# Performance work log

Hardware: AMD Instinct MI355X
Metric: run time of the kernel (lower is better)

Reference implementation:

```python
import jax, jax.numpy as jnp
import numpy as np

B, T, N = 16, 1000, 100
ENC, VOCAB, EMB, HID, ATT, PROJ = 512, 10025, 640, 1024, 1024, 1024


def setup_inputs() -> dict:
    key = jax.random.key(0)
    ks = jax.random.split(key, 20)
    g = lambda k, shape, s=0.02: (jax.random.normal(k, shape) * s).astype(jnp.float32)
    inp = {
        "encoder_outputs": jax.random.normal(ks[0], (B, T, ENC), dtype=jnp.float32),
        "labels": jax.random.randint(ks[1], (B, N), 0, VOCAB),
        "enc_seq_len": jax.random.randint(ks[2], (B,), T // 2, T + 1),
        # parameters (torch layout: Linear weight [out, in])
        "embed_table": g(ks[3], (VOCAB, EMB)),
        "W_ih": g(ks[4], (4 * HID, EMB + ENC)),
        "W_hh": g(ks[5], (4 * HID, HID)),
        "b_ih": jnp.zeros((4 * HID,), jnp.float32),
        "b_hh": jnp.zeros((4 * HID,), jnp.float32),
        "W_s": g(ks[6], (ATT, HID)),              # s_transformed, no bias
        "W_enc": g(ks[7], (ATT, ENC)),            # enc_ctx
        "b_enc": jnp.zeros((ATT,), jnp.float32),
        "v_att": g(ks[8], (ATT,)),                # attention energy vector
        "W_fert": g(ks[9], (ENC,)),               # inv_fertility [1,ENC] squeezed
        "W_fb": g(ks[10], (ATT,)),                # weight_feedback [ATT,1] squeezed
        "W_ro": g(ks[11], (PROJ, HID + EMB + ENC)),
        "b_ro": jnp.zeros((PROJ,), jnp.float32),
        "W_out": g(ks[12], (VOCAB, PROJ // 2)),
        "b_out": jnp.zeros((VOCAB,), jnp.float32),
    }
    return inp


def _decode(encoder_outputs, labels, enc_seq_len, embed_table, W_ih, W_hh, b_ih,
            b_hh, W_s, W_enc, b_enc, v_att, W_fert, W_fb, W_ro, b_ro, W_out, b_out):
    Bb, Tt, _ = encoder_outputs.shape
    # shifted target embeddings: pad one zero step at front, drop last -> [B,N,EMB]
    emb = embed_table[labels]
    emb = jnp.concatenate([jnp.zeros_like(emb[:, :1]), emb[:, :-1]], axis=1)

    enc_ctx = jnp.einsum("btd,ad->bta", encoder_outputs, W_enc) + b_enc  # [B,T,ATT]
    inv_fert = jax.nn.sigmoid(encoder_outputs @ W_fert)                   # [B,T]
    seq_mask = jnp.arange(Tt)[None, :] < enc_seq_len[:, None]             # [B,T]

    def step(carry, e_t):
        h, c, att_ctx, accum = carry  # h,c:[B,HID]  att_ctx:[B,ENC]  accum:[B,T]
        x = jnp.concatenate([e_t, att_ctx], axis=-1)
        gates = x @ W_ih.T + b_ih + h @ W_hh.T + b_hh
        i, f, gg, o = jnp.split(gates, 4, axis=-1)
        c_new = jax.nn.sigmoid(f) * c + jax.nn.sigmoid(i) * jnp.tanh(gg)
        h_new = jax.nn.sigmoid(o) * jnp.tanh(c_new)

        s_t = h_new @ W_s.T                                   # [B,ATT]
        wf = accum[:, :, None] * W_fb[None, None, :]          # [B,T,ATT]
        energies = jnp.tanh(enc_ctx + s_t[:, None, :] + wf) @ v_att  # [B,T]
        energies = jnp.where(seq_mask, energies, -jnp.inf)
        weights = jax.nn.softmax(energies, axis=1)            # [B,T]
        ctx = jnp.einsum("bt,btd->bd", weights, encoder_outputs)
        accum_new = accum + weights * inv_fert * 0.5
        return (h_new, c_new, ctx, accum_new), (h_new, ctx)

    carry0 = (
        jnp.zeros((Bb, HID), jnp.float32),
        jnp.zeros((Bb, HID), jnp.float32),
        jnp.zeros((Bb, ENC), jnp.float32),
        jnp.zeros((Bb, Tt), jnp.float32),
    )
    carry, (s_seq, ctx_seq) = jax.lax.scan(step, carry0, emb.transpose(1, 0, 2))
    s_stacked = s_seq.transpose(1, 0, 2)        # [B,N,HID]
    ctx_stacked = ctx_seq.transpose(1, 0, 2)    # [B,N,ENC]

    ro_in = jnp.concatenate([s_stacked, emb, ctx_stacked], axis=-1) @ W_ro.T + b_ro
    readout = jnp.max(ro_in.reshape(Bb, ro_in.shape[1], -1, 2), axis=-1)  # maxout
    logits = readout @ W_out.T + b_out
    return logits, carry


def reference(encoder_outputs, labels, enc_seq_len, embed_table, W_ih, W_hh, b_ih,
              b_hh, W_s, W_enc, b_enc, v_att, W_fert, W_fb, W_ro, b_ro, W_out, b_out):
    logits, (h, c, att_ctx, accum) = _decode(
        encoder_outputs, labels, enc_seq_len, embed_table, W_ih, W_hh, b_ih, b_hh,
        W_s, W_enc, b_enc, v_att, W_fert, W_fb, W_ro, b_ro, W_out, b_out)
    return logits, h, c, att_ctx, accum
```

## Files before the change

kernel.cpp:

```cpp
#include <hip/hip_runtime.h>
#include <math.h>

#define Bsz 16
#define Tsz 1000
#define Nsz 100
#define ENC 512
#define VOCAB 10025
#define EMB 640
#define HID 1024
#define ATT 1024
#define KX (EMB + ENC)
#define KRO (HID + EMB + ENC)

__device__ __forceinline__ float4 ld4(const float* p) { return *reinterpret_cast<const float4*>(p); }
__device__ __forceinline__ float dot4(float4 a, float4 b) { return a.x*b.x + a.y*b.y + a.z*b.z + a.w*b.w; }
__device__ __forceinline__ float sigmoidf_(float x) { return 1.f / (1.f + __expf(-x)); }
__device__ __forceinline__ float ftanh_(float x) {
    x = fminf(15.f, fmaxf(-15.f, x));
    float e = __expf(2.f * x);
    return (e - 1.f) / (e + 1.f);
}

__global__ __launch_bounds__(256) void k_init(float* accum) {
    int i = blockIdx.x * 256 + threadIdx.x;
    if (i < Bsz * Tsz) accum[i] = 0.f;
}

__global__ __launch_bounds__(256) void k_embed(const int* __restrict__ labels,
                                               const float* __restrict__ table,
                                               float* __restrict__ roA) {
    int idx = blockIdx.x * 256 + threadIdx.x;
    if (idx >= Bsz * Nsz * EMB) return;
    int e = idx % EMB;
    int bn = idx / EMB;
    int n = bn % Nsz, b = bn / Nsz;
    float v = 0.f;
    if (n > 0) {
        int lab = labels[b * Nsz + n - 1];
        v = table[(size_t)lab * EMB + e];
    }
    roA[(size_t)bn * KRO + HID + e] = v;
}

#define BM 64
#define BN 64
#define BK 16
template <int MAXOUT>
__global__ __launch_bounds__(256) void sgemm_nt(const float* __restrict__ A,
                                                const float* __restrict__ W,
                                                const float* __restrict__ bias,
                                                float* __restrict__ C,
                                                int M, int Nc, int K, int ldC) {
    __shared__ __align__(16) float As[BK][BM + 4];
    __shared__ __align__(16) float Ws[BK][BN + 4];
    int m0 = blockIdx.y * BM, n0 = blockIdx.x * BN;
    int tid = threadIdx.x;
    int tx = tid & 15, ty = tid >> 4;
    int lr = tid >> 2;
    int lk = (tid & 3) * 4;
    float acc[4][4] = {};
    for (int k0 = 0; k0 < K; k0 += BK) {
        {
            int m = m0 + lr;
            float4 v = (m < M) ? ld4(&A[(size_t)m * K + k0 + lk]) : float4{0.f, 0.f, 0.f, 0.f};
            As[lk + 0][lr] = v.x; As[lk + 1][lr] = v.y; As[lk + 2][lr] = v.z; As[lk + 3][lr] = v.w;
        }
        {
            int n = n0 + lr;
            float4 v = (n < Nc) ? ld4(&W[(size_t)n * K + k0 + lk]) : float4{0.f, 0.f, 0.f, 0.f};
            Ws[lk + 0][lr] = v.x; Ws[lk + 1][lr] = v.y; Ws[lk + 2][lr] = v.z; Ws[lk + 3][lr] = v.w;
        }
        __syncthreads();
#pragma unroll
        for (int k = 0; k < BK; k++) {
            float4 a = *reinterpret_cast<const float4*>(&As[k][ty * 4]);
            float4 w = *reinterpret_cast<const float4*>(&Ws[k][tx * 4]);
            acc[0][0] += a.x * w.x; acc[0][1] += a.x * w.y; acc[0][2] += a.x * w.z; acc[0][3] += a.x * w.w;
            acc[1][0] += a.y * w.x; acc[1][1] += a.y * w.y; acc[1][2] += a.y * w.z; acc[1][3] += a.y * w.w;
            acc[2][0] += a.z * w.x; acc[2][1] += a.z * w.y; acc[2][2] += a.z * w.z; acc[2][3] += a.z * w.w;
            acc[3][0] += a.w * w.x; acc[3][1] += a.w * w.y; acc[3][2] += a.w * w.z; acc[3][3] += a.w * w.w;
        }
        __syncthreads();
    }
#pragma unroll
    for (int i = 0; i < 4; i++) {
        int m = m0 + ty * 4 + i;
        if (m >= M) continue;
        if (MAXOUT) {
#pragma unroll
            for (int j = 0; j < 2; j++) {
                int n = n0 + tx * 4 + 2 * j;
                float v0 = acc[i][2 * j] + bias[n];
                float v1 = acc[i][2 * j + 1] + bias[n + 1];
                C[(size_t)m * ldC + n / 2] = fmaxf(v0, v1);
            }
        } else {
#pragma unroll
            for (int j = 0; j < 4; j++) {
                int n = n0 + tx * 4 + j;
                if (n < Nc) C[(size_t)m * ldC + n] = acc[i][j] + bias[n];
            }
        }
    }
}

__global__ __launch_bounds__(256) void k_ifert(const float* __restrict__ enc,
                                               const float* __restrict__ Wfert,
                                               float* __restrict__ ifert) {
    int wv = (blockIdx.x * 256 + threadIdx.x) >> 6;
    int lane = threadIdx.x & 63;
    if (wv >= Bsz * Tsz) return;
    const float* row = enc + (size_t)wv * ENC;
    float s = 0.f;
    for (int k = lane * 4; k < ENC; k += 256) s += dot4(ld4(row + k), ld4(Wfert + k));
    for (int o = 32; o; o >>= 1) s += __shfl_xor(s, o, 64);
    if (lane == 0) ifert[wv] = 1.f / (1.f + __expf(-s));
}

__global__ __launch_bounds__(256) void k_gates(float* __restrict__ roA, float* __restrict__ cbuf,
                                               const float* __restrict__ Wih, const float* __restrict__ Whh,
                                               const float* __restrict__ bih, const float* __restrict__ bhh,
                                               int t) {
    int wv = (blockIdx.x * 256 + threadIdx.x) >> 6;
    int lane = threadIdx.x & 63;
    int j = wv >> 1;
    int b0 = (wv & 1) << 3;
    float acc[4][8];
#pragma unroll
    for (int g = 0; g < 4; g++)
#pragma unroll
        for (int bb = 0; bb < 8; bb++) acc[g][bb] = 0.f;

    const float* wi0 = Wih + (size_t)(0 * HID + j) * KX;
    const float* wi1 = Wih + (size_t)(1 * HID + j) * KX;
    const float* wi2 = Wih + (size_t)(2 * HID + j) * KX;
    const float* wi3 = Wih + (size_t)(3 * HID + j) * KX;
    const float* wh0 = Whh + (size_t)(0 * HID + j) * HID;
    const float* wh1 = Whh + (size_t)(1 * HID + j) * HID;
    const float* wh2 = Whh + (size_t)(2 * HID + j) * HID;
    const float* wh3 = Whh + (size_t)(3 * HID + j) * HID;
    const float* xrow[8];
    const float* prow[8];
#pragma unroll
    for (int bb = 0; bb < 8; bb++) {
        xrow[bb] = roA + (size_t)((b0 + bb) * Nsz + t) * KRO;
        prow[bb] = roA + (size_t)((b0 + bb) * Nsz + (t - 1)) * KRO;
    }
    for (int k = lane * 4; k < EMB; k += 256) {
        float4 w0 = ld4(wi0 + k), w1 = ld4(wi1 + k), w2 = ld4(wi2 + k), w3 = ld4(wi3 + k);
#pragma unroll
        for (int bb = 0; bb < 8; bb++) {
            float4 x = ld4(xrow[bb] + HID + k);
            acc[0][bb] += dot4(w0, x); acc[1][bb] += dot4(w1, x);
            acc[2][bb] += dot4(w2, x); acc[3][bb] += dot4(w3, x);
        }
    }
    if (t > 0) {
        for (int k = lane * 4; k < ENC; k += 256) {
            float4 w0 = ld4(wi0 + EMB + k), w1 = ld4(wi1 + EMB + k), w2 = ld4(wi2 + EMB + k), w3 = ld4(wi3 + EMB + k);
#pragma unroll
            for (int bb = 0; bb < 8; bb++) {
                float4 x = ld4(prow[bb] + HID + EMB + k);
                acc[0][bb] += dot4(w0, x); acc[1][bb] += dot4(w1, x);
                acc[2][bb] += dot4(w2, x); acc[3][bb] += dot4(w3, x);
            }
        }
        for (int k = lane * 4; k < HID; k += 256) {
            float4 w0 = ld4(wh0 + k), w1 = ld4(wh1 + k), w2 = ld4(wh2 + k), w3 = ld4(wh3 + k);
#pragma unroll
            for (int bb = 0; bb < 8; bb++) {
                float4 x = ld4(prow[bb] + k);
                acc[0][bb] += dot4(w0, x); acc[1][bb] += dot4(w1, x);
                acc[2][bb] += dot4(w2, x); acc[3][bb] += dot4(w3, x);
            }
        }
    }
#pragma unroll
    for (int g = 0; g < 4; g++)
#pragma unroll
        for (int bb = 0; bb < 8; bb++) {
            float v = acc[g][bb];
            for (int o = 32; o; o >>= 1) v += __shfl_xor(v, o, 64);
            acc[g][bb] = v;
        }
    if (lane < 8) {
        int b = b0 + lane;
        float gi = acc[0][lane] + bih[j] + bhh[j];
        float gf = acc[1][lane] + bih[HID + j] + bhh[HID + j];
        float gg = acc[2][lane] + bih[2 * HID + j] + bhh[2 * HID + j];
        float go = acc[3][lane] + bih[3 * HID + j] + bhh[3 * HID + j];
        float cold = (t > 0) ? cbuf[b * HID + j] : 0.f;
        float cn = sigmoidf_(gf) * cold + sigmoidf_(gi) * ftanh_(gg);
        float hn = sigmoidf_(go) * ftanh_(cn);
        cbuf[b * HID + j] = cn;
        roA[(size_t)(b * Nsz + t) * KRO + j] = hn;
    }
}

__global__ __launch_bounds__(256) void k_s(const float* __restrict__ roA, const float* __restrict__ Wsm,
                                           float* __restrict__ st, int t) {
    int wv = (blockIdx.x * 256 + threadIdx.x) >> 6;
    int lane = threadIdx.x & 63;
    float acc[16];
#pragma unroll
    for (int b = 0; b < 16; b++) acc[b] = 0.f;
    const float* wr = Wsm + (size_t)wv * HID;
    const float* hrow[16];
#pragma unroll
    for (int b = 0; b < 16; b++) hrow[b] = roA + (size_t)(b * Nsz + t) * KRO;
    for (int k = lane * 4; k < HID; k += 256) {
        float4 w = ld4(wr + k);
#pragma unroll
        for (int b = 0; b < 16; b++) acc[b] += dot4(w, ld4(hrow[b] + k));
    }
#pragma unroll
    for (int b = 0; b < 16; b++) {
        float v = acc[b];
        for (int o = 32; o; o >>= 1) v += __shfl_xor(v, o, 64);
        acc[b] = v;
    }
    if (lane < 16) st[lane * ATT + wv] = acc[lane];
}

__global__ __launch_bounds__(256) void k_energy(const float* __restrict__ encctx,
                                                const float* __restrict__ st,
                                                const float* __restrict__ Wfb,
                                                const float* __restrict__ vatt,
                                                const float* __restrict__ accum,
                                                const int* __restrict__ seqlen,
                                                float* __restrict__ enw) {
    int wv = (blockIdx.x * 256 + threadIdx.x) >> 6;
    int lane = threadIdx.x & 63;
    int b = wv / Tsz, t = wv - b * Tsz;
    if (t >= seqlen[b]) {
        if (lane == 0) enw[wv] = -INFINITY;
        return;
    }
    float ac = accum[wv];
    const float* ec = encctx + (size_t)wv * ATT;
    const float* sr = st + b * ATT;
    float e = 0.f;
    for (int k = lane * 4; k < ATT; k += 256) {
        float4 c4 = ld4(ec + k), s4 = ld4(sr + k), f4 = ld4(Wfb + k), v4 = ld4(vatt + k);
        e += ftanh_(c4.x + s4.x + ac * f4.x) * v4.x;
        e += ftanh_(c4.y + s4.y + ac * f4.y) * v4.y;
        e += ftanh_(c4.z + s4.z + ac * f4.z) * v4.z;
        e += ftanh_(c4.w + s4.w + ac * f4.w) * v4.w;
    }
    for (int o = 32; o; o >>= 1) e += __shfl_xor(e, o, 64);
    if (lane == 0) enw[wv] = e;
}

__global__ __launch_bounds__(256) void k_softmax(float* __restrict__ enw, const float* __restrict__ ifert,
                                                 float* __restrict__ accum, float* __restrict__ roA,
                                                 const int* __restrict__ seqlen, int tstep) {
    int b = blockIdx.x, tid = threadIdx.x;
    __shared__ float redm[4], reds[4];
    int len = seqlen[b];
    float* row = enw + b * Tsz;
    float m = -INFINITY;
    for (int t = tid; t < len; t += 256) m = fmaxf(m, row[t]);
    for (int o = 32; o; o >>= 1) m = fmaxf(m, __shfl_xor(m, o, 64));
    if ((tid & 63) == 0) redm[tid >> 6] = m;
    __syncthreads();
    float M = fmaxf(fmaxf(redm[0], redm[1]), fmaxf(redm[2], redm[3]));
    float s = 0.f;
    for (int t = tid; t < len; t += 256) s += __expf(row[t] - M);
    for (int o = 32; o; o >>= 1) s += __shfl_xor(s, o, 64);
    if ((tid & 63) == 0) reds[tid >> 6] = s;
    __syncthreads();
    float inv = 1.f / (reds[0] + reds[1] + reds[2] + reds[3]);
    for (int t = tid; t < Tsz; t += 256) {
        float w = (t < len) ? __expf(row[t] - M) * inv : 0.f;
        row[t] = w;
        accum[b * Tsz + t] += w * ifert[b * Tsz + t] * 0.5f;
    }
    for (int d = tid; d < ENC; d += 256) roA[(size_t)(b * Nsz + tstep) * KRO + HID + EMB + d] = 0.f;
}

#define TCH 10
__global__ __launch_bounds__(256) void k_ctx(const float* __restrict__ enw, const float* __restrict__ enc,
                                             const int* __restrict__ seqlen, float* __restrict__ roA,
                                             int tstep) {
    int b = blockIdx.y;
    int tid = threadIdx.x;
    int len = seqlen[b];
    int t0 = blockIdx.x * (Tsz / TCH);
    int t1 = min(t0 + Tsz / TCH, len);
    if (t0 >= t1) return;
    float a0 = 0.f, a1 = 0.f;
    const float* w = enw + b * Tsz;
    for (int t = t0; t < t1; t++) {
        float wt = w[t];
        const float* er = enc + (size_t)(b * Tsz + t) * ENC;
        a0 += wt * er[tid];
        a1 += wt * er[tid + 256];
    }
    float* dst = roA + (size_t)(b * Nsz + tstep) * KRO + HID + EMB;
    atomicAdd(dst + tid, a0);
    atomicAdd(dst + tid + 256, a1);
}

__global__ __launch_bounds__(256) void k_final(const float* __restrict__ roA, const float* __restrict__ cbuf,
                                               const float* __restrict__ accum, float* __restrict__ out) {
    int idx = blockIdx.x * 256 + threadIdx.x;
    const int base = Bsz * Nsz * VOCAB;
    const int OH = Bsz * HID, OC = Bsz * HID, OA = Bsz * ENC, OAC = Bsz * Tsz;
    if (idx < OH) {
        int b = idx / HID, j = idx % HID;
        out[base + idx] = roA[(size_t)(b * Nsz + Nsz - 1) * KRO + j];
        return;
    }
    idx -= OH;
    if (idx < OC) { out[base + OH + idx] = cbuf[idx]; return; }
    idx -= OC;
    if (idx < OA) {
        int b = idx / ENC, d = idx % ENC;
        out[base + OH + OC + idx] = roA[(size_t)(b * Nsz + Nsz - 1) * KRO + HID + EMB + d];
        return;
    }
    idx -= OA;
    if (idx < OAC) out[base + OH + OC + OA + idx] = accum[idx];
}

extern "C" void kernel_launch(void* const* d_in, const int* in_sizes, int n_in,
                              void* d_out, int out_size, void* d_ws, size_t ws_size,
                              hipStream_t stream) {
    const float* enc   = (const float*)d_in[0];
    const int* labels  = (const int*)d_in[1];
    const int* seqlen  = (const int*)d_in[2];
    const float* table = (const float*)d_in[3];
    const float* Wih   = (const float*)d_in[4];
    const float* Whh   = (const float*)d_in[5];
    const float* bih   = (const float*)d_in[6];
    const float* bhh   = (const float*)d_in[7];
    const float* Wsm   = (const float*)d_in[8];
    const float* Wenc  = (const float*)d_in[9];
    const float* benc  = (const float*)d_in[10];
    const float* vatt  = (const float*)d_in[11];
    const float* Wfert = (const float*)d_in[12];
    const float* Wfb   = (const float*)d_in[13];
    const float* Wro   = (const float*)d_in[14];
    const float* bro   = (const float*)d_in[15];
    const float* Wout  = (const float*)d_in[16];
    const float* bout  = (const float*)d_in[17];
    float* out = (float*)d_out;

    float* ws = (float*)d_ws;
    float* roA    = ws;
    float* cbuf   = roA + (size_t)1600 * KRO;
    float* encctx = cbuf + Bsz * HID;
    float* ifert  = encctx + (size_t)Bsz * Tsz * ATT;
    float* accum  = ifert + Bsz * Tsz;
    float* enw    = accum + Bsz * Tsz;
    float* st     = enw + Bsz * Tsz;
    float* rmx    = st + Bsz * ATT;

    k_init<<<(Bsz * Tsz + 255) / 256, 256, 0, stream>>>(accum);
    k_embed<<<(Bsz * Nsz * EMB + 255) / 256, 256, 0, stream>>>(labels, table, roA);
    sgemm_nt<0><<<dim3(ATT / BN, (Bsz * Tsz) / BM), 256, 0, stream>>>(enc, Wenc, benc, encctx,
                                                                     Bsz * Tsz, ATT, ENC, ATT);
    k_ifert<<<(Bsz * Tsz * 64 + 255) / 256, 256, 0, stream>>>(enc, Wfert, ifert);

    for (int t = 0; t < Nsz; t++) {
        k_gates<<<512, 256, 0, stream>>>(roA, cbuf, Wih, Whh, bih, bhh, t);
        k_s<<<256, 256, 0, stream>>>(roA, Wsm, st, t);
        k_energy<<<(Bsz * Tsz * 64) / 256, 256, 0, stream>>>(encctx, st, Wfb, vatt, accum, seqlen, enw);
        k_softmax<<<Bsz, 256, 0, stream>>>(enw, ifert, accum, roA, seqlen, t);
        k_ctx<<<dim3(TCH, Bsz), 256, 0, stream>>>(enw, enc, seqlen, roA, t);
    }

    sgemm_nt<1><<<dim3(1024 / BN, 1600 / BM), 256, 0, stream>>>(roA, Wro, bro, rmx, 1600, 1024, KRO, 512);
    sgemm_nt<0><<<dim3((VOCAB + BN - 1) / BN, 1600 / BM), 256, 0, stream>>>(rmx, Wout, bout, out,
                                                                           1600, VOCAB, 512, VOCAB);
    k_final<<<(Bsz * HID * 2 + Bsz * ENC + Bsz * Tsz + 255) / 256, 256, 0, stream>>>(roA, cbuf, accum, out);
}
```

Baseline: 8.183 ms.

## Replace FP32 SIMT GEMMs with split-bf16 MFMA GEMMs

Replaces the scalar FP32 tiled GEMM used for the encoder context, readout maxout and output projection with a 128x128-tile MFMA kernel. Each FP32 operand is split into a high and a low bf16 part, and three bf16 MFMA products are summed to approximate FP32 accuracy. The intent is to move the large non-recurrent GEMMs onto matrix cores. The cost is conversion work in the load path, more LDS traffic, and a small loss of precision compared with true FP32.

After: 7.996 ms. 2.3% less time.

```diff
diff --git a/kernel.cpp b/kernel.cpp
--- a/kernel.cpp
+++ b/kernel.cpp
@@ -12,6 +12,10 @@
 #define KX (EMB + ENC)
 #define KRO (HID + EMB + ENC)
 
+typedef short s16x8 __attribute__((ext_vector_type(8)));
+typedef unsigned short u16x4 __attribute__((ext_vector_type(4)));
+typedef float f32x4 __attribute__((ext_vector_type(4)));
+
 __device__ __forceinline__ float4 ld4(const float* p) { return *reinterpret_cast<const float4*>(p); }
 __device__ __forceinline__ float dot4(float4 a, float4 b) { return a.x*b.x + a.y*b.y + a.z*b.z + a.w*b.w; }
 __device__ __forceinline__ float sigmoidf_(float x) { return 1.f / (1.f + __expf(-x)); }
@@ -19,6 +23,15 @@
     x = fminf(15.f, fmaxf(-15.f, x));
     float e = __expf(2.f * x);
     return (e - 1.f) / (e + 1.f);
+}
+__device__ __forceinline__ unsigned short f2bf(float x) {
+    union { float f; unsigned u; } v; v.f = x;
+    unsigned r = v.u + 0x7fffu + ((v.u >> 16) & 1u);
+    return (unsigned short)(r >> 16);
+}
+__device__ __forceinline__ float bf2f(unsigned short h) {
+    union { float f; unsigned u; } v; v.u = ((unsigned)h) << 16;
+    return v.f;
 }
 
 __global__ __launch_bounds__(256) void k_init(float* accum) {
@@ -42,63 +55,89 @@
     roA[(size_t)bn * KRO + HID + e] = v;
 }
 
-#define BM 64
-#define BN 64
-#define BK 16
-template <int MAXOUT>
-__global__ __launch_bounds__(256) void sgemm_nt(const float* __restrict__ A,
-                                                const float* __restrict__ W,
-                                                const float* __restrict__ bias,
-                                                float* __restrict__ C,
-                                                int M, int Nc, int K, int ldC) {
-    __shared__ __align__(16) float As[BK][BM + 4];
-    __shared__ __align__(16) float Ws[BK][BN + 4];
-    int m0 = blockIdx.y * BM, n0 = blockIdx.x * BN;
+template <int MODE>
+__global__ __launch_bounds__(256) void mfma_gemm(const float* __restrict__ A,
+                                                 const float* __restrict__ W,
+                                                 const float* __restrict__ bias,
+                                                 float* __restrict__ C,
+                                                 int M, int Nc, int K, int ldC) {
+    __shared__ unsigned short Ah[128][40], Al[128][40], Wh[128][40], Wl[128][40];
     int tid = threadIdx.x;
-    int tx = tid & 15, ty = tid >> 4;
-    int lr = tid >> 2;
-    int lk = (tid & 3) * 4;
-    float acc[4][4] = {};
-    for (int k0 = 0; k0 < K; k0 += BK) {
-        {
-            int m = m0 + lr;
-            float4 v = (m < M) ? ld4(&A[(size_t)m * K + k0 + lk]) : float4{0.f, 0.f, 0.f, 0.f};
-            As[lk + 0][lr] = v.x; As[lk + 1][lr] = v.y; As[lk + 2][lr] = v.z; As[lk + 3][lr] = v.w;
-        }
-        {
-            int n = n0 + lr;
-            float4 v = (n < Nc) ? ld4(&W[(size_t)n * K + k0 + lk]) : float4{0.f, 0.f, 0.f, 0.f};
-            Ws[lk + 0][lr] = v.x; Ws[lk + 1][lr] = v.y; Ws[lk + 2][lr] = v.z; Ws[lk + 3][lr] = v.w;
+    int lane = tid & 63;
+    int wave = tid >> 6;
+    int wm = (wave >> 1) * 64, wn = (wave & 1) * 64;
+    int m0 = blockIdx.y * 128, n0 = blockIdx.x * 128;
+    int lrow = tid >> 1;
+    int lcol = (tid & 1) * 16;
+    bool aval = (m0 + lrow) < M;
+    bool wval = (n0 + lrow) < Nc;
+    const float* Arow = A + (size_t)(m0 + lrow) * K + lcol;
+    const float* Wrow = W + (size_t)(n0 + lrow) * K + lcol;
+    int frow = lane & 15, fk = (lane >> 4) * 8;
+
+    f32x4 acc[4][4];
+#pragma unroll
+    for (int i = 0; i < 4; i++)
+#pragma unroll
+        for (int j = 0; j < 4; j++) acc[i][j] = (f32x4){0.f, 0.f, 0.f, 0.f};
+
+    const float4 z4 = {0.f, 0.f, 0.f, 0.f};
+    for (int k0 = 0; k0 < K; k0 += 32) {
+#pragma unroll
+        for (int c = 0; c < 16; c += 4) {
+            float4 av = aval ? ld4(Arow + k0 + c) : z4;
+            u16x4 hv, lv;
+            hv.x = f2bf(av.x); lv.x = f2bf(av.x - bf2f(hv.x));
+            hv.y = f2bf(av.y); lv.y = f2bf(av.y - bf2f(hv.y));
+            hv.z = f2bf(av.z); lv.z = f2bf(av.z - bf2f(hv.z));
+            hv.w = f2bf(av.w); lv.w = f2bf(av.w - bf2f(hv.w));
+            *(u16x4*)&Ah[lrow][lcol + c] = hv;
+            *(u16x4*)&Al[lrow][lcol + c] = lv;
+            float4 wv = wval ? ld4(Wrow + k0 + c) : z4;
+            hv.x = f2bf(wv.x); lv.x = f2bf(wv.x - bf2f(hv.x));
+            hv.y = f2bf(wv.y); lv.y = f2bf(wv.y - bf2f(hv.y));
+            hv.z = f2bf(wv.z); lv.z = f2bf(wv.z - bf2f(hv.z));
+            hv.w = f2bf(wv.w); lv.w = f2bf(wv.w - bf2f(hv.w));
+            *(u16x4*)&Wh[lrow][lcol + c] = hv;
+            *(u16x4*)&Wl[lrow][lcol + c] = lv;
         }
         __syncthreads();
-#pragma unroll
-        for (int k = 0; k < BK; k++) {
-            float4 a = *reinterpret_cast<const float4*>(&As[k][ty * 4]);
-            float4 w = *reinterpret_cast<const float4*>(&Ws[k][tx * 4]);
-            acc[0][0] += a.x * w.x; acc[0][1] += a.x * w.y; acc[0][2] += a.x * w.z; acc[0][3] += a.x * w.w;
-            acc[1][0] += a.y * w.x; acc[1][1] += a.y * w.y; acc[1][2] += a.y * w.z; acc[1][3] += a.y * w.w;
-            acc[2][0] += a.z * w.x; acc[2][1] += a.z * w.y; acc[2][2] += a.z * w.z; acc[2][3] += a.z * w.w;
-            acc[3][0] += a.w * w.x; acc[3][1] += a.w * w.y; acc[3][2] += a.w * w.z; acc[3][3] += a.w * w.w;
-        }
+        s16x8 afh[4], afl[4], bfh[4], bfl[4];
+#pragma unroll
+        for (int i = 0; i < 4; i++) {
+            afh[i] = *(const s16x8*)&Ah[wm + i * 16 + frow][fk];
+            afl[i] = *(const s16x8*)&Al[wm + i * 16 + frow][fk];
+            bfh[i] = *(const s16x8*)&Wh[wn + i * 16 + frow][fk];
+            bfl[i] = *(const s16x8*)&Wl[wn + i * 16 + frow][fk];
+        }
+#pragma unroll
+        for (int mi = 0; mi < 4; mi++)
+#pragma unroll
+            for (int ni = 0; ni < 4; ni++) {
+                acc[mi][ni] = __builtin_amdgcn_mfma_f32_16x16x32_bf16(afh[mi], bfh[ni], acc[mi][ni], 0, 0, 0);
+                acc[mi][ni] = __builtin_amdgcn_mfma_f32_16x16x32_bf16(afl[mi], bfh[ni], acc[mi][ni], 0, 0, 0);
+                acc[mi][ni] = __builtin_amdgcn_mfma_f32_16x16x32_bf16(afh[mi], bfl[ni], acc[mi][ni], 0, 0, 0);
+            }
         __syncthreads();
     }
-#pragma unroll
-    for (int i = 0; i < 4; i++) {
-        int m = m0 + ty * 4 + i;
-        if (m >= M) continue;
-        if (MAXOUT) {
-#pragma unroll
-            for (int j = 0; j < 2; j++) {
-                int n = n0 + tx * 4 + 2 * j;
-                float v0 = acc[i][2 * j] + bias[n];
-                float v1 = acc[i][2 * j + 1] + bias[n + 1];
-                C[(size_t)m * ldC + n / 2] = fmaxf(v0, v1);
-            }
-        } else {
-#pragma unroll
-            for (int j = 0; j < 4; j++) {
-                int n = n0 + tx * 4 + j;
-                if (n < Nc) C[(size_t)m * ldC + n] = acc[i][j] + bias[n];
+    int crb = (lane >> 4) * 4;
+    int ccol = lane & 15;
+#pragma unroll
+    for (int mi = 0; mi < 4; mi++) {
+#pragma unroll
+        for (int r = 0; r < 4; r++) {
+            int m = m0 + wm + mi * 16 + crb + r;
+#pragma unroll
+            for (int ni = 0; ni < 4; ni++) {
+                int n = n0 + wn + ni * 16 + ccol;
+                if (MODE == 0) {
+                    if (m < M && n < Nc) C[(size_t)m * ldC + n] = acc[mi][ni][r] + bias[n];
+                } else {
+                    float v = (n < Nc) ? acc[mi][ni][r] + bias[n] : -INFINITY;
+                    float o = __shfl_xor(v, 1, 64);
+                    if (((lane & 1) == 0) && m < M && n < Nc)
+                        C[(size_t)m * ldC + (n >> 1)] = fmaxf(v, o);
+                }
             }
         }
     }
@@ -358,8 +397,8 @@
 
     k_init<<<(Bsz * Tsz + 255) / 256, 256, 0, stream>>>(accum);
     k_embed<<<(Bsz * Nsz * EMB + 255) / 256, 256, 0, stream>>>(labels, table, roA);
-    sgemm_nt<0><<<dim3(ATT / BN, (Bsz * Tsz) / BM), 256, 0, stream>>>(enc, Wenc, benc, encctx,
-                                                                     Bsz * Tsz, ATT, ENC, ATT);
+    mfma_gemm<0><<<dim3(ATT / 128, (Bsz * Tsz) / 128), 256, 0, stream>>>(enc, Wenc, benc, encctx,
+                                                                        Bsz * Tsz, ATT, ENC, ATT);
     k_ifert<<<(Bsz * Tsz * 64 + 255) / 256, 256, 0, stream>>>(enc, Wfert, ifert);
 
     for (int t = 0; t < Nsz; t++) {
@@ -370,8 +409,9 @@
         k_ctx<<<dim3(TCH, Bsz), 256, 0, stream>>>(enw, enc, seqlen, roA, t);
     }
 
-    sgemm_nt<1><<<dim3(1024 / BN, 1600 / BM), 256, 0, stream>>>(roA, Wro, bro, rmx, 1600, 1024, KRO, 512);
-    sgemm_nt<0><<<dim3((VOCAB + BN - 1) / BN, 1600 / BM), 256, 0, stream>>>(rmx, Wout, bout, out,
-                                                                           1600, VOCAB, 512, VOCAB);
+    mfma_gemm<1><<<dim3(1024 / 128, (1600 + 127) / 128), 256, 0, stream>>>(roA, Wro, bro, rmx,
+                                                                          1600, 1024, KRO, 512);
+    mfma_gemm<0><<<dim3((VOCAB + 127) / 128, (1600 + 127) / 128), 256, 0, stream>>>(rmx, Wout, bout, out,
+                                                                                   1600, VOCAB, 512, VOCAB);
     k_final<<<(Bsz * HID * 2 + Bsz * ENC + Bsz * Tsz + 255) / 256, 256, 0, stream>>>(roA, cbuf, accum, out);
 }
```
